# Kernel tuning notes

Measured on AMD Instinct MI355X. Metric: run time of the kernel, lower is better.

Reference implementation:

```python
import jax, jax.numpy as jnp
import numpy as np

B = 1024      # graphs per batch
N = 64        # nodes per graph
DEG = 8       # edges per node
E = B * N * DEG
V = 52737     # vocab (different_ids)
D = 512       # embed / hidden dim
K1, K2, K3 = 52, 42, 34  # ceil(0.8*64), ceil(0.8*52), ceil(0.8*42)


def setup_inputs() -> dict:
    key = jax.random.key(0)
    ks = jax.random.split(key, 40)
    x_ids = jax.random.randint(ks[0], (B * N,), 0, V)
    off = jnp.repeat(jnp.arange(B) * N, N * DEG)  # graph offsets per edge
    edge_src = jax.random.randint(ks[1], (E,), 0, N) + off
    edge_dst = jax.random.randint(ks[2], (E,), 0, N) + off

    def lin(k, i, o):
        return jax.random.normal(k, (i, o), jnp.float32) / np.float32(np.sqrt(i))

    inp = dict(x_ids=x_ids, edge_src=edge_src, edge_dst=edge_dst)
    inp['emb'] = jax.random.normal(ks[3], (V, D), jnp.float32)
    # SAGEConv params: w*l/b*l act on aggregated neighbors, w*r on root
    for i, (kl, kr) in enumerate([(4, 5), (6, 7), (8, 9)], start=1):
        inp[f'w{i}l'] = lin(ks[kl], D, D)
        inp[f'b{i}l'] = jnp.zeros((D,), jnp.float32)
        inp[f'w{i}r'] = lin(ks[kr], D, D)
    # TopKPooling score vectors
    inp['p1'] = jax.random.normal(ks[10], (D,), jnp.float32)
    inp['p2'] = jax.random.normal(ks[11], (D,), jnp.float32)
    inp['p3'] = jax.random.normal(ks[12], (D,), jnp.float32)
    dims = [(1024, 512), (512, 256), (256, 128), (128, 64), (64, 1)]
    for i, (di, do) in enumerate(dims, start=1):
        inp[f'lw{i}'] = lin(ks[12 + i], di, do)
        inp[f'lb{i}'] = jnp.zeros((do,), jnp.float32)
    return inp


def _sage(x, src, dst, emask, wl, bl, wr):
    # PyG SAGEConv: mean-aggregate neighbor messages (src -> dst), plus root term
    n = x.shape[0]
    msg = x[src] * emask[:, None]
    s = jax.ops.segment_sum(msg, dst, num_segments=n)
    c = jax.ops.segment_sum(emask, dst, num_segments=n)
    agg = s / jnp.maximum(c, 1.0)[:, None]  # empty neighborhoods -> 0
    return agg @ wl + bl + x @ wr


def _topk_pool(x, src, dst, emask, w, k):
    # PyG TopKPooling: score = tanh(x.w / ||w||); keep top-k per graph, gate x
    n = x.shape[0]
    n_per = n // B
    score = jnp.tanh((x @ w) / jnp.linalg.norm(w))
    _, idx = jax.lax.top_k(score.reshape(B, n_per), k)      # [B, k] local ids
    perm = (idx + jnp.arange(B)[:, None] * n_per).reshape(-1)  # global ids
    x_new = x[perm] * score[perm][:, None]
    new_id = jnp.full((n,), -1, jnp.int32).at[perm].set(jnp.arange(B * k, dtype=jnp.int32))
    ns, nd = new_id[src], new_id[dst]
    valid = emask * (ns >= 0) * (nd >= 0)
    ns = jnp.where(valid > 0, ns, 0)
    nd = jnp.where(valid > 0, nd, 0)
    return x_new, ns, nd, valid.astype(x.dtype)


def _readout(x, k):
    xg = x.reshape(B, k, -1)
    return jnp.concatenate([xg.max(axis=1), xg.mean(axis=1)], axis=1)  # [B, 2F]


def _forward(x_ids, edge_src, edge_dst, emb,
             w1l, b1l, w1r, w2l, b2l, w2r, w3l, b3l, w3r,
             p1, p2, p3,
             lw1, lb1, lw2, lb2, lw3, lb3, lw4, lb4, lw5, lb5):
    x = emb[x_ids]                                  # [B*N, D]
    src, dst = edge_src, edge_dst
    emask = jnp.ones((E,), x.dtype)

    x = jax.nn.relu(_sage(x, src, dst, emask, w1l, b1l, w1r))
    x, src, dst, emask = _topk_pool(x, src, dst, emask, p1, K1)
    x1 = _readout(x, K1)

    x = jax.nn.relu(_sage(x, src, dst, emask, w2l, b2l, w2r))
    x, src, dst, emask = _topk_pool(x, src, dst, emask, p2, K2)
    x2 = _readout(x, K2)

    x = jax.nn.relu(_sage(x, src, dst, emask, w3l, b3l, w3r))
    x, src, dst, emask = _topk_pool(x, src, dst, emask, p3, K3)
    x3 = _readout(x, K3)

    h = x1 + x2 + x3                                # [B, 1024]
    h = jax.nn.relu(h @ lw1 + lb1)
    h = jax.nn.relu(h @ lw2 + lb2)
    h = jax.nn.relu(h @ lw3 + lb3)
    h = jax.nn.relu(h @ lw4 + lb4)
    # dropout p=0.5 is identity in eval mode
    return jax.nn.sigmoid(h @ lw5 + lb5)[:, 0]      # [B]


def reference(x_ids, edge_src, edge_dst, emb,
              w1l, b1l, w1r, w2l, b2l, w2r, w3l, b3l, w3r,
              p1, p2, p3,
              lw1, lb1, lw2, lb2, lw3, lb3, lw4, lb4, lw5, lb5):
    return _forward(x_ids, edge_src, edge_dst, emb,
                    w1l, b1l, w1r, w2l, b2l, w2r, w3l, b3l, w3r,
                    p1, p2, p3,
                    lw1, lb1, lw2, lb2, lw3, lb3, lw4, lb4, lw5, lb5)
```

## Files before the change

### kernel.cpp

```cpp
#include <hip/hip_runtime.h>
#include <math.h>

#define BG 1024
#define EPG 512
#define ETOT (BG*EPG)
#define DIM 512
#define KP1 52
#define KP2 42
#define KP3 34

typedef unsigned int uint;
typedef short s16x8 __attribute__((ext_vector_type(8)));
typedef float f32x4 __attribute__((ext_vector_type(4)));

__device__ __forceinline__ unsigned short f2b(float x) {
    uint u = __float_as_uint(x);
    u = u + 0x7fffu + ((u >> 16) & 1u);
    return (unsigned short)(u >> 16);
}
__device__ __forceinline__ float b2f(unsigned short h) {
    return __uint_as_float(((uint)h) << 16);
}
__device__ __forceinline__ void splitf(float x, unsigned short& h, unsigned short& l) {
    h = f2b(x);
    l = f2b(x - b2f(h));
}
__device__ __forceinline__ uint pk2(unsigned short a, unsigned short b) {
    return (uint)a | ((uint)b << 16);
}

__device__ __forceinline__ void gload16(const void* g, void* l) {
    __builtin_amdgcn_global_load_lds(
        (const __attribute__((address_space(1))) void*)g,
        (__attribute__((address_space(3))) void*)l, 16, 0, 0);
}

__global__ void __launch_bounds__(256)
gather_split(const int* __restrict__ ids, const float* __restrict__ emb,
             unsigned short* __restrict__ Xhi, unsigned short* __restrict__ Xlo)
{
    int tid = blockIdx.x * 256 + threadIdx.x;
    int row = tid >> 6;
    int c8  = (tid & 63) * 8;
    const float4* s = (const float4*)(emb + (size_t)ids[row] * DIM + c8);
    float4 v0 = s[0], v1 = s[1];
    float vs[8] = {v0.x,v0.y,v0.z,v0.w,v1.x,v1.y,v1.z,v1.w};
    unsigned short h[8], l[8];
#pragma unroll
    for (int i = 0; i < 8; ++i) splitf(vs[i], h[i], l[i]);
    uint4 H, L;
    H.x = pk2(h[0],h[1]); H.y = pk2(h[2],h[3]); H.z = pk2(h[4],h[5]); H.w = pk2(h[6],h[7]);
    L.x = pk2(l[0],l[1]); L.y = pk2(l[2],l[3]); L.z = pk2(l[4],l[5]); L.w = pk2(l[6],l[7]);
    *(uint4*)(Xhi + (size_t)row * DIM + c8) = H;
    *(uint4*)(Xlo + (size_t)row * DIM + c8) = L;
}

struct WPtrs { const float* w[6]; };

__global__ void __launch_bounds__(256)
split_wT_all(WPtrs p, unsigned short* __restrict__ WT)
{
    const int wi = blockIdx.x >> 8;
    const int bb = blockIdx.x & 255;
    const float* W = p.w[wi];
    unsigned short* Thi = WT + (size_t)(2 * wi) * DIM * DIM;
    unsigned short* Tlo = Thi + (size_t)DIM * DIM;
    __shared__ float tl[32][33];
    const int t  = threadIdx.x;
    const int bx = bb & 15;
    const int by = bb >> 4;
    const int lx = t & 31, ly = t >> 5;
    for (int r = ly; r < 32; r += 8)
        tl[r][lx] = W[(size_t)(by*32 + r) * DIM + bx*32 + lx];
    __syncthreads();
    for (int r = ly; r < 32; r += 8) {
        float v = tl[lx][r];
        unsigned short h, l; splitf(v, h, l);
        size_t o = (size_t)(bx*32 + r) * DIM + by*32 + lx;
        Thi[o] = h; Tlo[o] = l;
    }
}

template<int NPER>
__global__ void __launch_bounds__(256, 4)
agg_lds4(const unsigned short* __restrict__ Xhi, const unsigned short* __restrict__ Xlo,
         const int* __restrict__ esrc, const int* __restrict__ edst,
         const float* __restrict__ emask,
         unsigned short* __restrict__ Ghi, unsigned short* __restrict__ Glo)
{
    const int g  = blockIdx.x >> 2;
    const int c0 = (blockIdx.x & 3) * 128;
    const int t  = threadIdx.x;
    __shared__ __align__(16) unsigned short xs[NPER * 256];
    __shared__ int ldst[EPG];
    __shared__ int lsrc[EPG];
    __shared__ int ssrc[EPG];
    __shared__ int cnt4[4][64];
    __shared__ int offs[NPER + 1];

    for (int s = t; s < NPER * 32; s += 256) {
        const int row  = s >> 5;
        const int half = (s >> 4) & 1;
        const int c8   = (s & 15) * 8;
        const unsigned short* src =
            (half ? Xlo : Xhi) + (size_t)(g * NPER + row) * DIM + c0 + c8;
        gload16(src, (char*)xs + (size_t)s * 16);
    }
    const int eb = g * EPG;
    for (int e = t; e < EPG; e += 256) {
        float m = emask ? emask[eb + e] : 1.0f;
        ldst[e] = (m > 0.f) ? (edst[eb + e] - g * NPER) : -1;
        lsrc[e] = esrc[eb + e] - g * NPER;
    }
    __syncthreads();
    {
        const int d = t & 63, q = t >> 6;
        int c = 0;
        for (int e = q * 128; e < q * 128 + 128; ++e) c += (ldst[e] == d);
        cnt4[q][d] = c;
    }
    __syncthreads();
    if (t == 0) {
        int s = 0;
        for (int i = 0; i < NPER; ++i) {
            offs[i] = s;
            s += cnt4[0][i] + cnt4[1][i] + cnt4[2][i] + cnt4[3][i];
        }
        offs[NPER] = s;
    }
    __syncthreads();
    {
        const int d = t & 63, q = t >> 6;
        if (d < NPER) {
            int w = offs[d];
            for (int q2 = 0; q2 < q; ++q2) w += cnt4[q2][d];
            for (int e = q * 128; e < q * 128 + 128; ++e)
                if (ldst[e] == d) ssrc[w++] = lsrc[e];
        }
    }
    __syncthreads();
    const int ch = (t & 31) * 4;
    const int d0 = t >> 5;
    for (int d = d0; d < NPER; d += 8) {
        const int cA = offs[d], cB = offs[d + 1];
        float s0 = 0.f, s1 = 0.f, s2 = 0.f, s3 = 0.f;
        for (int j = cA; j < cB; ++j) {
            const int base = ssrc[j] * 256 + ch;
            ushort4 h = *(const ushort4*)&xs[base];
            ushort4 l = *(const ushort4*)&xs[base + 128];
            s0 += b2f(h.x) + b2f(l.x);
            s1 += b2f(h.y) + b2f(l.y);
            s2 += b2f(h.z) + b2f(l.z);
            s3 += b2f(h.w) + b2f(l.w);
        }
        const float den = fmaxf((float)(cB - cA), 1.0f);
        s0 /= den; s1 /= den; s2 /= den; s3 /= den;
        unsigned short h0,h1,h2,h3,l0,l1,l2,l3;
        splitf(s0,h0,l0); splitf(s1,h1,l1); splitf(s2,h2,l2); splitf(s3,h3,l3);
        const size_t wo = (size_t)(g * NPER + d) * DIM + c0 + ch;
        *(uint2*)(Ghi + wo) = make_uint2(pk2(h0,h1), pk2(h2,h3));
        *(uint2*)(Glo + wo) = make_uint2(pk2(l0,l1), pk2(l2,l3));
    }
}

__global__ void __launch_bounds__(256)
gemm_sage(const unsigned short* __restrict__ Ghi, const unsigned short* __restrict__ Glo,
          const unsigned short* __restrict__ WLhi, const unsigned short* __restrict__ WLlo,
          const unsigned short* __restrict__ Xhi, const unsigned short* __restrict__ Xlo,
          const unsigned short* __restrict__ WRhi, const unsigned short* __restrict__ WRlo,
          const float* __restrict__ bias, float* __restrict__ C, int M)
{
    __shared__ unsigned short sA[128 * 64];
    __shared__ unsigned short sW[128 * 64];

    const int t = threadIdx.x;
    const uint nwg = gridDim.x;
    const uint q8  = nwg >> 3;
    const uint bid = blockIdx.x;
    const uint sw  = (bid & 7) * q8 + (bid >> 3);
    const int  m0  = (int)(sw >> 2) * 128;
    const int  n0  = (int)(sw & 3) * 128;

    const int l  = t & 63;
    const int w  = t >> 6;
    const int wr = w >> 1;
    const int wc = w & 1;
    const int lr = l & 15;
    const int lq = l >> 4;

    f32x4 acc[4][4];
#pragma unroll
    for (int i = 0; i < 4; ++i)
#pragma unroll
        for (int j = 0; j < 4; ++j) acc[i][j] = (f32x4){0.f, 0.f, 0.f, 0.f};

    uint srow[4], soff[4];
#pragma unroll
    for (int i = 0; i < 4; ++i) {
        uint p = (uint)i * 256u + (uint)t;
        uint row = p >> 3, pc = p & 7;
        srow[i] = row;
        soff[i] = (pc ^ (row & 7u)) * 8u;
    }

#pragma unroll 1
    for (int s = 0; s < 6; ++s) {
        const int src = (s >= 3) ? 1 : 0;
        const int combo = s - src * 3;
        const unsigned short* Ap = src ? ((combo == 2) ? Xlo : Xhi)
                                       : ((combo == 2) ? Glo : Ghi);
        const unsigned short* Wp = src ? ((combo == 1) ? WRlo : WRhi)
                                       : ((combo == 1) ? WLlo : WLhi);
#pragma unroll 1
        for (int kt = 0; kt < 8; ++kt) {
            const int kb = kt * 64;
#pragma unroll
            for (int i = 0; i < 4; ++i) {
                const unsigned short* ga =
                    Ap + (size_t)(m0 + srow[i]) * DIM + kb + soff[i];
                const unsigned short* gw =
                    Wp + (size_t)(n0 + srow[i]) * DIM + kb + soff[i];
                uint p16 = ((uint)i * 256u + (uint)t) * 16u;
                gload16(ga, (char*)sA + p16);
                gload16(gw, (char*)sW + p16);
            }
            __syncthreads();
#pragma unroll
            for (int ks = 0; ks < 2; ++ks) {
                s16x8 af[4], wf[4];
#pragma unroll
                for (int i = 0; i < 4; ++i) {
                    int arow = wr * 64 + i * 16 + lr;
                    int off = arow * 128 + 16 * ((ks * 4 + lq) ^ (arow & 7));
                    af[i] = *(const s16x8*)((const char*)sA + off);
                }
#pragma unroll
                for (int j = 0; j < 4; ++j) {
                    int wrow = wc * 64 + j * 16 + lr;
                    int off = wrow * 128 + 16 * ((ks * 4 + lq) ^ (wrow & 7));
                    wf[j] = *(const s16x8*)((const char*)sW + off);
                }
#pragma unroll
                for (int i = 0; i < 4; ++i)
#pragma unroll
                    for (int j = 0; j < 4; ++j)
                        acc[i][j] = __builtin_amdgcn_mfma_f32_16x16x32_bf16(
                            af[i], wf[j], acc[i][j], 0, 0, 0);
            }
            __syncthreads();
        }
    }

#pragma unroll
    for (int i = 0; i < 4; ++i) {
        const int r0 = m0 + wr * 64 + i * 16 + lq * 4;
#pragma unroll
        for (int j = 0; j < 4; ++j) {
            const int cc = n0 + wc * 64 + j * 16 + lr;
            const float bv = bias[cc];
#pragma unroll
            for (int r = 0; r < 4; ++r) {
                float v = acc[i][j][r] + bv;
                C[(size_t)(r0 + r) * DIM + cc] = fmaxf(v, 0.f);
            }
        }
    }
}

template<int NPER, int KEEP, bool REMAP, bool INIT>
__global__ void __launch_bounds__(256)
pool_fused(const float* __restrict__ Y, const float* __restrict__ p,
           unsigned short* __restrict__ Xhi, unsigned short* __restrict__ Xlo,
           const int* __restrict__ es, const int* __restrict__ ed,
           const float* __restrict__ em,
           int* __restrict__ nes, int* __restrict__ ned, float* __restrict__ nem,
           float* __restrict__ H)
{
    const int g = blockIdx.x;
    const int t = threadIdx.x;
    const int wave = t >> 6, lane = t & 63;
    __shared__ float ssc[NPER];
    __shared__ float spnorm;
    __shared__ int   perm[KEEP];
    __shared__ float sgate[KEEP];
    __shared__ int   lnewid[NPER];

    if (wave == 0) {
        float v = 0.f;
#pragma unroll
        for (int i = 0; i < 8; ++i) { float x = p[lane + i * 64]; v = fmaf(x, x, v); }
#pragma unroll
        for (int off = 32; off; off >>= 1) v += __shfl_down(v, off);
        if (lane == 0) spnorm = sqrtf(v);
    }
    for (int nl = wave; nl < NPER; nl += 4) {
        const float* yr = Y + (size_t)(g * NPER + nl) * DIM;
        float v = 0.f;
#pragma unroll
        for (int i = 0; i < 8; ++i) v = fmaf(yr[lane + i * 64], p[lane + i * 64], v);
#pragma unroll
        for (int off = 32; off; off >>= 1) v += __shfl_down(v, off);
        if (lane == 0) ssc[nl] = v;
    }
    __syncthreads();
    float s = 0.f;
    if (t < NPER) s = tanhf(ssc[t] / spnorm);
    __syncthreads();
    if (t < NPER) ssc[t] = s;
    __syncthreads();
    if (t < NPER) {
        int r = 0;
        for (int j = 0; j < NPER; ++j) {
            float sj = ssc[j];
            r += (sj > s) || (sj == s && j < t);
        }
        lnewid[t] = (r < KEEP) ? (g * KEEP + r) : -1;
        if (r < KEEP) { perm[r] = t; sgate[r] = s; }
    }
    __syncthreads();

    float mx0 = -1e30f, mx1 = -1e30f, sm0 = 0.f, sm1 = 0.f;
    for (int r = 0; r < KEEP; ++r) {
        const float2 v = ((const float2*)(Y + (size_t)(g * NPER + perm[r]) * DIM))[t];
        const float sv = sgate[r];
        float a = v.x * sv, b = v.y * sv;
        mx0 = fmaxf(mx0, a); mx1 = fmaxf(mx1, b);
        sm0 += a; sm1 += b;
        unsigned short ha, la, hb, lb;
        splitf(a, ha, la); splitf(b, hb, lb);
        size_t o = (size_t)(g * KEEP + r) * DIM + 2 * t;
        *(uint*)(Xhi + o) = pk2(ha, hb);
        *(uint*)(Xlo + o) = pk2(la, lb);
    }
    {
        const size_t o = (size_t)g * 1024;
        const float me0 = sm0 / (float)KEEP, me1 = sm1 / (float)KEEP;
        if (INIT) {
            H[o + 2*t]       = mx0; H[o + 2*t + 1]       = mx1;
            H[o + 512 + 2*t] = me0; H[o + 512 + 2*t + 1] = me1;
        } else {
            H[o + 2*t]       += mx0; H[o + 2*t + 1]       += mx1;
            H[o + 512 + 2*t] += me0; H[o + 512 + 2*t + 1] += me1;
        }
    }

    if (REMAP) {
        const int eb = g * EPG;
        for (int e = t; e < EPG; e += 256) {
            const float m = em ? em[eb + e] : 1.f;
            int sN = -1, dN = -1;
            if (m > 0.f) {
                sN = lnewid[es[eb + e] - g * NPER];
                dN = lnewid[ed[eb + e] - g * NPER];
            }
            const bool v = (m > 0.f) && (sN >= 0) && (dN >= 0);
            nes[eb + e] = v ? sN : 0;
            ned[eb + e] = v ? dN : 0;
            nem[eb + e] = v ? 1.f : 0.f;
        }
    }
}

__global__ void __launch_bounds__(256)
mlp_fused(const float* __restrict__ H,
          const float* __restrict__ lw1, const float* __restrict__ lb1,
          const float* __restrict__ lw2, const float* __restrict__ lb2,
          const float* __restrict__ lw3, const float* __restrict__ lb3,
          const float* __restrict__ lw4, const float* __restrict__ lb4,
          const float* __restrict__ lw5, const float* __restrict__ lb5,
          float* __restrict__ out)
{
    __shared__ float h0[2][1024];
    __shared__ float y1[2][512];
    __shared__ float y2[2][256];
    __shared__ float y3[2][128];
    __shared__ float y4[2][64];
    const int t = threadIdx.x;
    const int r0 = blockIdx.x * 2;

    {
        float4 a = *(const float4*)&H[(size_t)r0 * 1024 + t * 4];
        float4 b = *(const float4*)&H[(size_t)(r0 + 1) * 1024 + t * 4];
        *(float4*)&h0[0][t * 4] = a;
        *(float4*)&h0[1][t * 4] = b;
    }
    __syncthreads();
    {
        float a00 = 0.f, a01 = 0.f, a10 = 0.f, a11 = 0.f;
        const int c = t * 2;
#pragma unroll 4
        for (int k = 0; k < 1024; ++k) {
            float2 wv = *(const float2*)&lw1[(size_t)k * 512 + c];
            float x0 = h0[0][k], x1 = h0[1][k];
            a00 = fmaf(x0, wv.x, a00); a01 = fmaf(x0, wv.y, a01);
            a10 = fmaf(x1, wv.x, a10); a11 = fmaf(x1, wv.y, a11);
        }
        y1[0][c]     = fmaxf(a00 + lb1[c], 0.f);
        y1[0][c + 1] = fmaxf(a01 + lb1[c + 1], 0.f);
        y1[1][c]     = fmaxf(a10 + lb1[c], 0.f);
        y1[1][c + 1] = fmaxf(a11 + lb1[c + 1], 0.f);
    }
    __syncthreads();
    {
        float a0 = 0.f, a1 = 0.f;
#pragma unroll 4
        for (int k = 0; k < 512; ++k) {
            float wv = lw2[(size_t)k * 256 + t];
            a0 = fmaf(y1[0][k], wv, a0);
            a1 = fmaf(y1[1][k], wv, a1);
        }
        y2[0][t] = fmaxf(a0 + lb2[t], 0.f);
        y2[1][t] = fmaxf(a1 + lb2[t], 0.f);
    }
    __syncthreads();
    if (t < 128) {
        float a0 = 0.f, a1 = 0.f;
#pragma unroll 4
        for (int k = 0; k < 256; ++k) {
            float wv = lw3[(size_t)k * 128 + t];
            a0 = fmaf(y2[0][k], wv, a0);
            a1 = fmaf(y2[1][k], wv, a1);
        }
        y3[0][t] = fmaxf(a0 + lb3[t], 0.f);
        y3[1][t] = fmaxf(a1 + lb3[t], 0.f);
    }
    __syncthreads();
    if (t < 64) {
        float a0 = 0.f, a1 = 0.f;
#pragma unroll 4
        for (int k = 0; k < 128; ++k) {
            float wv = lw4[(size_t)k * 64 + t];
            a0 = fmaf(y3[0][k], wv, a0);
            a1 = fmaf(y3[1][k], wv, a1);
        }
        y4[0][t] = fmaxf(a0 + lb4[t], 0.f);
        y4[1][t] = fmaxf(a1 + lb4[t], 0.f);
    }
    __syncthreads();
    const int wv = t >> 6, ln = t & 63;
    if (wv < 2) {
        float v = y4[wv][ln] * lw5[ln];
#pragma unroll
        for (int off = 32; off; off >>= 1) v += __shfl_down(v, off);
        if (ln == 0) out[r0 + wv] = 1.f / (1.f + expf(-(v + lb5[0])));
    }
}

extern "C" void kernel_launch(void* const* d_in, const int* in_sizes, int n_in,
                              void* d_out, int out_size, void* d_ws, size_t ws_size,
                              hipStream_t stream)
{
    const int*   x_ids = (const int*)d_in[0];
    const int*   esrc  = (const int*)d_in[1];
    const int*   edst  = (const int*)d_in[2];
    const float* emb   = (const float*)d_in[3];
    const float* w1l = (const float*)d_in[4],  *b1l = (const float*)d_in[5],  *w1r = (const float*)d_in[6];
    const float* w2l = (const float*)d_in[7],  *b2l = (const float*)d_in[8],  *w2r = (const float*)d_in[9];
    const float* w3l = (const float*)d_in[10], *b3l = (const float*)d_in[11], *w3r = (const float*)d_in[12];
    const float* p1  = (const float*)d_in[13];
    const float* p2  = (const float*)d_in[14];
    const float* p3  = (const float*)d_in[15];
    const float* lw1 = (const float*)d_in[16], *lb1 = (const float*)d_in[17];
    const float* lw2 = (const float*)d_in[18], *lb2 = (const float*)d_in[19];
    const float* lw3 = (const float*)d_in[20], *lb3 = (const float*)d_in[21];
    const float* lw4 = (const float*)d_in[22], *lb4 = (const float*)d_in[23];
    const float* lw5 = (const float*)d_in[24], *lb5 = (const float*)d_in[25];
    float* out = (float*)d_out;

    const size_t PL = (size_t)65536 * DIM;
    unsigned short* Xhi = (unsigned short*)d_ws;
    unsigned short* Xlo = Xhi + PL;
    unsigned short* Ghi = Xlo + PL;
    unsigned short* Glo = Ghi + PL;
    float* Cc = (float*)(Glo + PL);
    float* H  = Cc + PL;
    int*   ES2 = (int*)(H + (size_t)1024 * 1024);
    int*   ED2 = ES2 + ETOT;
    float* EM2 = (float*)(ED2 + ETOT);
    int*   ES3 = (int*)(EM2 + ETOT);
    int*   ED3 = ES3 + ETOT;
    float* EM3 = (float*)(ED3 + ETOT);
    unsigned short* WT = (unsigned short*)(EM3 + ETOT);
    const size_t WSZ = (size_t)DIM * DIM;
    unsigned short *w1lh = WT + 0*WSZ,  *w1ll = WT + 1*WSZ;
    unsigned short *w1rh = WT + 2*WSZ,  *w1rl = WT + 3*WSZ;
    unsigned short *w2lh = WT + 4*WSZ,  *w2ll = WT + 5*WSZ;
    unsigned short *w2rh = WT + 6*WSZ,  *w2rl = WT + 7*WSZ;
    unsigned short *w3lh = WT + 8*WSZ,  *w3ll = WT + 9*WSZ;
    unsigned short *w3rh = WT + 10*WSZ, *w3rl = WT + 11*WSZ;

    WPtrs wp;
    wp.w[0] = w1l; wp.w[1] = w1r; wp.w[2] = w2l;
    wp.w[3] = w2r; wp.w[4] = w3l; wp.w[5] = w3r;
    split_wT_all<<<6 * 256, 256, 0, stream>>>(wp, WT);

    gather_split<<<16384, 256, 0, stream>>>(x_ids, emb, Xhi, Xlo);
    agg_lds4<64><<<BG * 4, 256, 0, stream>>>(Xhi, Xlo, esrc, edst, nullptr, Ghi, Glo);
    gemm_sage<<<(65536/128)*4, 256, 0, stream>>>(Ghi, Glo, w1lh, w1ll,
                                                 Xhi, Xlo, w1rh, w1rl, b1l, Cc, 65536);
    pool_fused<64, KP1, true, true><<<BG, 256, 0, stream>>>(
        Cc, p1, Xhi, Xlo, esrc, edst, nullptr, ES2, ED2, EM2, H);

    agg_lds4<KP1><<<BG * 4, 256, 0, stream>>>(Xhi, Xlo, ES2, ED2, EM2, Ghi, Glo);
    gemm_sage<<<(53248/128)*4, 256, 0, stream>>>(Ghi, Glo, w2lh, w2ll,
                                                 Xhi, Xlo, w2rh, w2rl, b2l, Cc, 53248);
    pool_fused<KP1, KP2, true, false><<<BG, 256, 0, stream>>>(
        Cc, p2, Xhi, Xlo, ES2, ED2, EM2, ES3, ED3, EM3, H);

    agg_lds4<KP2><<<BG * 4, 256, 0, stream>>>(Xhi, Xlo, ES3, ED3, EM3, Ghi, Glo);
    gemm_sage<<<(43008/128)*4, 256, 0, stream>>>(Ghi, Glo, w3lh, w3ll,
                                                 Xhi, Xlo, w3rh, w3rl, b3l, Cc, 43008);
    pool_fused<KP2, KP3, false, false><<<BG, 256, 0, stream>>>(
        Cc, p3, Xhi, Xlo, nullptr, nullptr, nullptr, nullptr, nullptr, nullptr, H);

    mlp_fused<<<512, 256, 0, stream>>>(H, lw1, lb1, lw2, lb2, lw3, lb3,
                                       lw4, lb4, lw5, lb5, out);
}
```

Before: 1.306 ms.

## Presort edges per graph once and fuse pool scoring into GEMM epilogue

Edges are counting-sorted by destination once per graph into packed (dst<<16|src) lists with offsets. Each pooling stage then remaps and re-sorts only the surviving edges, so the aggregation kernels no longer redo the per-block count/scan/scatter and no longer reread the mask arrays; four aggregation blocks per graph previously repeated that sort. The TopK score dot product x·p is computed in the SAGE GEMM epilogue as per-column-tile partial sums, which removes a full reread of the activation matrix in the pool kernel. The cost is an extra sort kernel, a shuffle reduction and an extra block-level sync in the GEMM epilogue, and more shared memory in the pool kernel.

```diff
diff --git a/kernel.cpp b/kernel.cpp
--- a/kernel.cpp
+++ b/kernel.cpp
@@ -8,6 +8,7 @@
 #define KP1 52
 #define KP2 42
 #define KP3 34
+#define OFS 80
 
 typedef unsigned int uint;
 typedef short s16x8 __attribute__((ext_vector_type(8)));
@@ -81,21 +82,59 @@
     }
 }
 
+__global__ void __launch_bounds__(256)
+sort_edges1(const int* __restrict__ esrc, const int* __restrict__ edst,
+            uint* __restrict__ SE, int* __restrict__ OF)
+{
+    const int g = blockIdx.x;
+    const int t = threadIdx.x;
+    __shared__ int ld[EPG];
+    __shared__ int ls[EPG];
+    __shared__ int cnt4[4][64];
+    __shared__ int offs[65];
+    const int eb = g * EPG;
+    for (int e = t; e < EPG; e += 256) {
+        ld[e] = edst[eb + e] - g * 64;
+        ls[e] = esrc[eb + e] - g * 64;
+    }
+    __syncthreads();
+    {
+        const int d = t & 63, q = t >> 6;
+        int c = 0;
+        for (int e = q * 128; e < q * 128 + 128; ++e) c += (ld[e] == d);
+        cnt4[q][d] = c;
+    }
+    __syncthreads();
+    if (t == 0) {
+        int s = 0;
+        for (int i = 0; i < 64; ++i) {
+            offs[i] = s;
+            s += cnt4[0][i] + cnt4[1][i] + cnt4[2][i] + cnt4[3][i];
+        }
+        offs[64] = s;
+    }
+    __syncthreads();
+    {
+        const int d = t & 63, q = t >> 6;
+        int w = offs[d];
+        for (int q2 = 0; q2 < q; ++q2) w += cnt4[q2][d];
+        for (int e = q * 128; e < q * 128 + 128; ++e)
+            if (ld[e] == d) SE[(size_t)g * EPG + (w++)] = ((uint)d << 16) | (uint)ls[e];
+    }
+    if (t <= 64) OF[g * OFS + t] = offs[t];
+}
+
 template<int NPER>
 __global__ void __launch_bounds__(256, 4)
-agg_lds4(const unsigned short* __restrict__ Xhi, const unsigned short* __restrict__ Xlo,
-         const int* __restrict__ esrc, const int* __restrict__ edst,
-         const float* __restrict__ emask,
-         unsigned short* __restrict__ Ghi, unsigned short* __restrict__ Glo)
+agg_sorted(const unsigned short* __restrict__ Xhi, const unsigned short* __restrict__ Xlo,
+           const uint* __restrict__ SE, const int* __restrict__ OF,
+           unsigned short* __restrict__ Ghi, unsigned short* __restrict__ Glo)
 {
     const int g  = blockIdx.x >> 2;
     const int c0 = (blockIdx.x & 3) * 128;
     const int t  = threadIdx.x;
     __shared__ __align__(16) unsigned short xs[NPER * 256];
-    __shared__ int ldst[EPG];
-    __shared__ int lsrc[EPG];
-    __shared__ int ssrc[EPG];
-    __shared__ int cnt4[4][64];
+    __shared__ uint el[EPG];
     __shared__ int offs[NPER + 1];
 
     for (int s = t; s < NPER * 32; s += 256) {
@@ -106,46 +145,19 @@
             (half ? Xlo : Xhi) + (size_t)(g * NPER + row) * DIM + c0 + c8;
         gload16(src, (char*)xs + (size_t)s * 16);
     }
-    const int eb = g * EPG;
-    for (int e = t; e < EPG; e += 256) {
-        float m = emask ? emask[eb + e] : 1.0f;
-        ldst[e] = (m > 0.f) ? (edst[eb + e] - g * NPER) : -1;
-        lsrc[e] = esrc[eb + e] - g * NPER;
-    }
-    __syncthreads();
-    {
-        const int d = t & 63, q = t >> 6;
-        int c = 0;
-        for (int e = q * 128; e < q * 128 + 128; ++e) c += (ldst[e] == d);
-        cnt4[q][d] = c;
-    }
-    __syncthreads();
-    if (t == 0) {
-        int s = 0;
-        for (int i = 0; i < NPER; ++i) {
-            offs[i] = s;
-            s += cnt4[0][i] + cnt4[1][i] + cnt4[2][i] + cnt4[3][i];
-        }
-        offs[NPER] = s;
-    }
-    __syncthreads();
-    {
-        const int d = t & 63, q = t >> 6;
-        if (d < NPER) {
-            int w = offs[d];
-            for (int q2 = 0; q2 < q; ++q2) w += cnt4[q2][d];
-            for (int e = q * 128; e < q * 128 + 128; ++e)
-                if (ldst[e] == d) ssrc[w++] = lsrc[e];
-        }
-    }
-    __syncthreads();
+    if (t <= NPER) offs[t] = OF[g * OFS + t];
+    __syncthreads();
+    const int cnt = offs[NPER];
+    for (int e = t; e < cnt; e += 256) el[e] = SE[(size_t)g * EPG + e];
+    __syncthreads();
+
     const int ch = (t & 31) * 4;
     const int d0 = t >> 5;
     for (int d = d0; d < NPER; d += 8) {
         const int cA = offs[d], cB = offs[d + 1];
         float s0 = 0.f, s1 = 0.f, s2 = 0.f, s3 = 0.f;
         for (int j = cA; j < cB; ++j) {
-            const int base = ssrc[j] * 256 + ch;
+            const int base = (int)(el[j] & 0xffffu) * 256 + ch;
             ushort4 h = *(const ushort4*)&xs[base];
             ushort4 l = *(const ushort4*)&xs[base + 128];
             s0 += b2f(h.x) + b2f(l.x);
@@ -168,10 +180,12 @@
           const unsigned short* __restrict__ WLhi, const unsigned short* __restrict__ WLlo,
           const unsigned short* __restrict__ Xhi, const unsigned short* __restrict__ Xlo,
           const unsigned short* __restrict__ WRhi, const unsigned short* __restrict__ WRlo,
-          const float* __restrict__ bias, float* __restrict__ C, int M)
+          const float* __restrict__ bias, const float* __restrict__ pvec,
+          float* __restrict__ C, float* __restrict__ SC4, int M)
 {
     __shared__ unsigned short sA[128 * 64];
     __shared__ unsigned short sW[128 * 64];
+    __shared__ float scp[128][2];
 
     const int t = threadIdx.x;
     const uint nwg = gridDim.x;
@@ -251,6 +265,12 @@
         }
     }
 
+    float part[4][4];
+#pragma unroll
+    for (int i = 0; i < 4; ++i)
+#pragma unroll
+        for (int r = 0; r < 4; ++r) part[i][r] = 0.f;
+
 #pragma unroll
     for (int i = 0; i < 4; ++i) {
         const int r0 = m0 + wr * 64 + i * 16 + lq * 4;
@@ -258,22 +278,41 @@
         for (int j = 0; j < 4; ++j) {
             const int cc = n0 + wc * 64 + j * 16 + lr;
             const float bv = bias[cc];
+            const float pv = pvec[cc];
 #pragma unroll
             for (int r = 0; r < 4; ++r) {
-                float v = acc[i][j][r] + bv;
-                C[(size_t)(r0 + r) * DIM + cc] = fmaxf(v, 0.f);
+                float v = fmaxf(acc[i][j][r] + bv, 0.f);
+                C[(size_t)(r0 + r) * DIM + cc] = v;
+                part[i][r] = fmaf(v, pv, part[i][r]);
             }
         }
     }
+#pragma unroll
+    for (int o = 1; o < 16; o <<= 1)
+#pragma unroll
+        for (int i = 0; i < 4; ++i)
+#pragma unroll
+            for (int r = 0; r < 4; ++r)
+                part[i][r] += __shfl_xor(part[i][r], o);
+    if (lr == 0) {
+#pragma unroll
+        for (int i = 0; i < 4; ++i)
+#pragma unroll
+            for (int r = 0; r < 4; ++r)
+                scp[wr * 64 + i * 16 + lq * 4 + r][wc] = part[i][r];
+    }
+    __syncthreads();
+    if (t < 128)
+        SC4[(size_t)(m0 + t) * 4 + (n0 >> 7)] = scp[t][0] + scp[t][1];
 }
 
 template<int NPER, int KEEP, bool REMAP, bool INIT>
 __global__ void __launch_bounds__(256)
 pool_fused(const float* __restrict__ Y, const float* __restrict__ p,
+           const float* __restrict__ SC4,
            unsigned short* __restrict__ Xhi, unsigned short* __restrict__ Xlo,
-           const int* __restrict__ es, const int* __restrict__ ed,
-           const float* __restrict__ em,
-           int* __restrict__ nes, int* __restrict__ ned, float* __restrict__ nem,
+           const uint* __restrict__ SEp, const int* __restrict__ OFp,
+           uint* __restrict__ SEn, int* __restrict__ OFn,
            float* __restrict__ H)
 {
     const int g = blockIdx.x;
@@ -284,6 +323,10 @@
     __shared__ int   perm[KEEP];
     __shared__ float sgate[KEEP];
     __shared__ int   lnewid[NPER];
+    __shared__ uint  eprev[EPG];
+    __shared__ uint  enew[EPG];
+    __shared__ int   cnt4[4][64];
+    __shared__ int   offs[KEEP + 1];
 
     if (wave == 0) {
         float v = 0.f;
@@ -293,28 +336,21 @@
         for (int off = 32; off; off >>= 1) v += __shfl_down(v, off);
         if (lane == 0) spnorm = sqrtf(v);
     }
-    for (int nl = wave; nl < NPER; nl += 4) {
-        const float* yr = Y + (size_t)(g * NPER + nl) * DIM;
-        float v = 0.f;
-#pragma unroll
-        for (int i = 0; i < 8; ++i) v = fmaf(yr[lane + i * 64], p[lane + i * 64], v);
-#pragma unroll
-        for (int off = 32; off; off >>= 1) v += __shfl_down(v, off);
-        if (lane == 0) ssc[nl] = v;
-    }
-    __syncthreads();
-    float s = 0.f;
-    if (t < NPER) s = tanhf(ssc[t] / spnorm);
-    __syncthreads();
-    if (t < NPER) ssc[t] = s;
     __syncthreads();
     if (t < NPER) {
+        const float* s4 = SC4 + (size_t)(g * NPER + t) * 4;
+        float raw = s4[0] + s4[1] + s4[2] + s4[3];
+        ssc[t] = tanhf(raw / spnorm);
+    }
+    __syncthreads();
+    if (t < NPER) {
+        const float s = ssc[t];
         int r = 0;
         for (int j = 0; j < NPER; ++j) {
             float sj = ssc[j];
             r += (sj > s) || (sj == s && j < t);
         }
-        lnewid[t] = (r < KEEP) ? (g * KEEP + r) : -1;
+        lnewid[t] = (r < KEEP) ? r : -1;
         if (r < KEEP) { perm[r] = t; sgate[r] = s; }
     }
     __syncthreads();
@@ -344,20 +380,50 @@
         }
     }
 
-    if (REMAP) {
-        const int eb = g * EPG;
-        for (int e = t; e < EPG; e += 256) {
-            const float m = em ? em[eb + e] : 1.f;
-            int sN = -1, dN = -1;
-            if (m > 0.f) {
-                sN = lnewid[es[eb + e] - g * NPER];
-                dN = lnewid[ed[eb + e] - g * NPER];
+    if constexpr (REMAP) {
+        const int cntp = OFp[g * OFS + NPER];
+        for (int e = t; e < cntp; e += 256)
+            eprev[e] = SEp[(size_t)g * EPG + e];
+        __syncthreads();
+        for (int e = t; e < cntp; e += 256) {
+            const uint pk = eprev[e];
+            const int ns = lnewid[pk & 0xffffu];
+            const int nd = lnewid[pk >> 16];
+            enew[e] = (ns >= 0 && nd >= 0)
+                ? (((uint)nd << 16) | (uint)ns) : 0xFFFFFFFFu;
+        }
+        __syncthreads();
+        {
+            const int d = t & 63, q = t >> 6;
+            int c = 0;
+            const int e0 = q * 128;
+            const int e1 = (e0 + 128 < cntp) ? e0 + 128 : cntp;
+            for (int e = e0; e < e1; ++e) c += ((enew[e] >> 16) == (uint)d);
+            cnt4[q][d] = c;
+        }
+        __syncthreads();
+        if (t == 0) {
+            int s = 0;
+            for (int i = 0; i < KEEP; ++i) {
+                offs[i] = s;
+                s += cnt4[0][i] + cnt4[1][i] + cnt4[2][i] + cnt4[3][i];
             }
-            const bool v = (m > 0.f) && (sN >= 0) && (dN >= 0);
-            nes[eb + e] = v ? sN : 0;
-            ned[eb + e] = v ? dN : 0;
-            nem[eb + e] = v ? 1.f : 0.f;
-        }
+            offs[KEEP] = s;
+        }
+        __syncthreads();
+        {
+            const int d = t & 63, q = t >> 6;
+            if (d < KEEP) {
+                int w = offs[d];
+                for (int q2 = 0; q2 < q; ++q2) w += cnt4[q2][d];
+                const int e0 = q * 128;
+                const int e1 = (e0 + 128 < cntp) ? e0 + 128 : cntp;
+                for (int e = e0; e < e1; ++e)
+                    if ((enew[e] >> 16) == (uint)d)
+                        SEn[(size_t)g * EPG + (w++)] = enew[e];
+            }
+        }
+        if (t <= KEEP) OFn[g * OFS + t] = offs[t];
     }
 }
 
@@ -472,15 +538,16 @@
     unsigned short* Xlo = Xhi + PL;
     unsigned short* Ghi = Xlo + PL;
     unsigned short* Glo = Ghi + PL;
-    float* Cc = (float*)(Glo + PL);
-    float* H  = Cc + PL;
-    int*   ES2 = (int*)(H + (size_t)1024 * 1024);
-    int*   ED2 = ES2 + ETOT;
-    float* EM2 = (float*)(ED2 + ETOT);
-    int*   ES3 = (int*)(EM2 + ETOT);
-    int*   ED3 = ES3 + ETOT;
-    float* EM3 = (float*)(ED3 + ETOT);
-    unsigned short* WT = (unsigned short*)(EM3 + ETOT);
+    float* Cc  = (float*)(Glo + PL);
+    float* H   = Cc + PL;
+    float* SC4 = H + (size_t)1024 * 1024;
+    uint*  SE1 = (uint*)(SC4 + (size_t)65536 * 4);
+    uint*  SE2 = SE1 + ETOT;
+    uint*  SE3 = SE2 + ETOT;
+    int*   OF1 = (int*)(SE3 + ETOT);
+    int*   OF2 = OF1 + BG * OFS;
+    int*   OF3 = OF2 + BG * OFS;
+    unsigned short* WT = (unsigned short*)(OF3 + BG * OFS);
     const size_t WSZ = (size_t)DIM * DIM;
     unsigned short *w1lh = WT + 0*WSZ,  *w1ll = WT + 1*WSZ;
     unsigned short *w1rh = WT + 2*WSZ,  *w1rl = WT + 3*WSZ;
@@ -495,23 +562,27 @@
     split_wT_all<<<6 * 256, 256, 0, stream>>>(wp, WT);
 
     gather_split<<<16384, 256, 0, stream>>>(x_ids, emb, Xhi, Xlo);
-    agg_lds4<64><<<BG * 4, 256, 0, stream>>>(Xhi, Xlo, esrc, edst, nullptr, Ghi, Glo);
+    sort_edges1<<<BG, 256, 0, stream>>>(esrc, edst, SE1, OF1);
+    agg_sorted<64><<<BG * 4, 256, 0, stream>>>(Xhi, Xlo, SE1, OF1, Ghi, Glo);
     gemm_sage<<<(65536/128)*4, 256, 0, stream>>>(Ghi, Glo, w1lh, w1ll,
-                                                 Xhi, Xlo, w1rh, w1rl, b1l, Cc, 65536);
+                                                 Xhi, Xlo, w1rh, w1rl,
+                                                 b1l, p1, Cc, SC4, 65536);
     pool_fused<64, KP1, true, true><<<BG, 256, 0, stream>>>(
-        Cc, p1, Xhi, Xlo, esrc, edst, nullptr, ES2, ED2, EM2, H);
-
-    agg_lds4<KP1><<<BG * 4, 256, 0, stream>>>(Xhi, Xlo, ES2, ED2, EM2, Ghi, Glo);
+        Cc, p1, SC4, Xhi, Xlo, SE1, OF1, SE2, OF2, H);
+
+    agg_sorted<KP1><<<BG * 4, 256, 0, stream>>>(Xhi, Xlo, SE2, OF2, Ghi, Glo);
     gemm_sage<<<(53248/128)*4, 256, 0, stream>>>(Ghi, Glo, w2lh, w2ll,
-                                                 Xhi, Xlo, w2rh, w2rl, b2l, Cc, 53248);
+                                                 Xhi, Xlo, w2rh, w2rl,
+                                                 b2l, p2, Cc, SC4, 53248);
     pool_fused<KP1, KP2, true, false><<<BG, 256, 0, stream>>>(
-        Cc, p2, Xhi, Xlo, ES2, ED2, EM2, ES3, ED3, EM3, H);
-
-    agg_lds4<KP2><<<BG * 4, 256, 0, stream>>>(Xhi, Xlo, ES3, ED3, EM3, Ghi, Glo);
+        Cc, p2, SC4, Xhi, Xlo, SE2, OF2, SE3, OF3, H);
+
+    agg_sorted<KP2><<<BG * 4, 256, 0, stream>>>(Xhi, Xlo, SE3, OF3, Ghi, Glo);
     gemm_sage<<<(43008/128)*4, 256, 0, stream>>>(Ghi, Glo, w3lh, w3ll,
-                                                 Xhi, Xlo, w3rh, w3rl, b3l, Cc, 43008);
+                                                 Xhi, Xlo, w3rh, w3rl,
+                                                 b3l, p3, Cc, SC4, 43008);
     pool_fused<KP2, KP3, false, false><<<BG, 256, 0, stream>>>(
-        Cc, p3, Xhi, Xlo, nullptr, nullptr, nullptr, nullptr, nullptr, nullptr, H);
+        Cc, p3, SC4, Xhi, Xlo, nullptr, nullptr, nullptr, nullptr, H);
 
     mlp_fused<<<512, 256, 0, stream>>>(H, lw1, lb1, lw2, lb2, lw3, lb3,
                                        lw4, lb4, lw5, lb5, out);
```

Result: faster. 1.170 ms (-10.4%).
